# Optimization experiments

Measured on AMD Instinct MI355X. Metric: run time of the kernel, lower is better.

## Reference

```python
import jax, jax.numpy as jnp
import numpy as np

EPS = 1e-5  # nn.LayerNorm default
H = 16      # n_heads

def _ln(x, s, b):
    m = x.mean(-1, keepdims=True)
    v = x.var(-1, keepdims=True)
    return (x - m) / jnp.sqrt(v + EPS) * s + b


def setup_inputs() -> dict:
    key = jax.random.key(0)
    B, T, D, L, V = 2, 1024, 1024, 6, 32000
    ks = jax.random.split(key, 10)
    def n(k, shape):
        return jax.random.normal(k, shape, dtype=jnp.float32) * 0.02
    return dict(
        x=jax.random.randint(ks[0], (B, T), 0, V),
        tok_emb=n(ks[1], (V, D)),
        pos_emb=n(ks[2], (T, D)),
        Wq=n(ks[3], (L, D, D)), bq=jnp.zeros((L, D), jnp.float32),
        Wk=n(ks[4], (L, D, D)), bk=jnp.zeros((L, D), jnp.float32),
        Wv=n(ks[5], (L, D, D)), bv=jnp.zeros((L, D), jnp.float32),
        ln1_s=jnp.ones((L, D), jnp.float32), ln1_b=jnp.zeros((L, D), jnp.float32),
        W1=n(ks[6], (L, D, 4 * D)), b1=jnp.zeros((L, 4 * D), jnp.float32),
        W2=n(ks[7], (L, 4 * D, D)), b2=jnp.zeros((L, D), jnp.float32),
        ln2_s=jnp.ones((L, D), jnp.float32), ln2_b=jnp.zeros((L, D), jnp.float32),
        Wout=n(ks[8], (D, V)), bout=jnp.zeros((V,), jnp.float32),
    )


def reference(x, tok_emb, pos_emb, Wq, bq, Wk, bk, Wv, bv, ln1_s, ln1_b,
              W1, b1, W2, b2, ln2_s, ln2_b, Wout, bout):
    B, T = x.shape
    D = tok_emb.shape[1]
    hd = D // H
    # embeddings (dropout = identity in eval)
    h = tok_emb[x] + pos_emb[:T]
    # additive causal mask: +1.0 on allowed (tril ones kept), -inf elsewhere,
    # exactly matching torch's tril-ones masked_fill mask
    tril = jnp.tril(jnp.ones((T, T), dtype=h.dtype))
    mask = jnp.where(tril == 0, -jnp.inf, 1.0).astype(h.dtype)
    scale = jnp.asarray(1.0 / np.sqrt(hd), h.dtype)

    def block(h, p):
        wq, bq_, wk, bk_, wv, bv_, l1s, l1b, w1, b1_, w2, b2_, l2s, l2b = p
        def heads(W, b):  # [B,T,D] -> [B,H,T,hd]
            return (h @ W + b).reshape(B, T, H, hd).transpose(0, 2, 1, 3)
        q, k, v = heads(wq, bq_), heads(wk, bk_), heads(wv, bv_)
        s = jnp.einsum('bhqd,bhkd->bhqk', q, k) * scale + mask
        a = jax.nn.softmax(s, axis=-1)
        o = jnp.einsum('bhqk,bhkd->bhqd', a, v).transpose(0, 2, 1, 3).reshape(B, T, D)
        hi = _ln(o + h, l1s, l1b)
        f = jax.nn.relu(hi @ w1 + b1_) @ w2 + b2_
        return _ln(f + hi, l2s, l2b), None

    h, _ = jax.lax.scan(block, h, (Wq, bq, Wk, bk, Wv, bv, ln1_s, ln1_b,
                                   W1, b1, W2, b2, ln2_s, ln2_b))
    return h @ Wout + bout
```

## Files before the change

kernel.cpp:

```cpp
#include <hip/hip_runtime.h>
#include <cstdint>
#include <cstddef>

typedef short bf16x8 __attribute__((ext_vector_type(8)));
typedef float f32x4 __attribute__((ext_vector_type(4)));
typedef unsigned short us4 __attribute__((ext_vector_type(4)));

#define DEV static __device__ __forceinline__

DEV unsigned short f2bf(float f) {
  union { float f; unsigned u; } v; v.f = f;
  unsigned r = v.u + 0x7FFFu + ((v.u >> 16) & 1u);
  return (unsigned short)(r >> 16);
}

DEV void gll16(const void* g, void* l) {
  __builtin_amdgcn_global_load_lds((const __attribute__((address_space(1))) void*)g,
                                   (__attribute__((address_space(3))) void*)l,
                                   16, 0, 0);
}

__global__ __launch_bounds__(256) void embed_kernel(
    const int* __restrict__ x, const float* __restrict__ te,
    const float* __restrict__ pe, float* __restrict__ hf,
    unsigned short* __restrict__ hb) {
  int row = blockIdx.x;
  int t = row & 1023;
  int tok = x[row];
  int tid = threadIdx.x;
  float4 v = ((const float4*)(te + (size_t)tok * 1024))[tid];
  float4 p = ((const float4*)(pe + (size_t)t * 1024))[tid];
  v.x += p.x; v.y += p.y; v.z += p.z; v.w += p.w;
  ((float4*)(hf + (size_t)row * 1024))[tid] = v;
  us4 bv; bv[0] = f2bf(v.x); bv[1] = f2bf(v.y); bv[2] = f2bf(v.z); bv[3] = f2bf(v.w);
  ((us4*)(hb + (size_t)row * 1024))[tid] = bv;
}

__global__ __launch_bounds__(256) void wconv_kernel(
    const float* __restrict__ W, unsigned short* __restrict__ Wt, int K, int N) {
  __shared__ float tile[32][33];
  int n0 = blockIdx.x * 32, k0 = blockIdx.y * 32;
  int tx = threadIdx.x & 31, ty = threadIdx.x >> 5;
#pragma unroll
  for (int i = 0; i < 4; ++i)
    tile[ty * 4 + i][tx] = W[(size_t)(k0 + ty * 4 + i) * N + n0 + tx];
  __syncthreads();
#pragma unroll
  for (int i = 0; i < 4; ++i)
    Wt[(size_t)(n0 + ty * 4 + i) * K + k0 + tx] = f2bf(tile[tx][ty * 4 + i]);
}

__global__ __launch_bounds__(256) void wconv5_kernel(
    const float* __restrict__ Wqf, const float* __restrict__ Wkf,
    const float* __restrict__ Wvf, const float* __restrict__ W1f,
    const float* __restrict__ W2f, unsigned short* __restrict__ wsc) {
  __shared__ float tile[32][33];
  const int bid = blockIdx.x;
  const float* W; unsigned short* Wt; int K, N, b;
  if (bid < 3072) {
    const int s = bid >> 10; b = bid & 1023;
    W = s == 0 ? Wqf : (s == 1 ? Wkf : Wvf);
    Wt = wsc + (size_t)s * 1048576; K = 1024; N = 1024;
  } else if (bid < 7168) {
    b = bid - 3072; W = W1f; Wt = wsc + 3145728; K = 1024; N = 4096;
  } else {
    b = bid - 7168; W = W2f; Wt = wsc + 7340032; K = 4096; N = 1024;
  }
  const int nb = N >> 5;
  const int n0 = (b & (nb - 1)) * 32, k0 = (b / nb) * 32;
  const int tx = threadIdx.x & 31, ty = threadIdx.x >> 5;
#pragma unroll
  for (int i = 0; i < 4; ++i)
    tile[ty * 4 + i][tx] = W[(size_t)(k0 + ty * 4 + i) * N + n0 + tx];
  __syncthreads();
#pragma unroll
  for (int i = 0; i < 4; ++i)
    Wt[(size_t)(n0 + ty * 4 + i) * K + k0 + tx] = f2bf(tile[tx][ty * 4 + i]);
}

template <int EPI>
__global__ __launch_bounds__(512) void gemm5_kernel(
    const unsigned short* __restrict__ A, const unsigned short* __restrict__ Bt,
    const float* __restrict__ bias1, const float* __restrict__ bias2,
    const float* __restrict__ bias3, void* __restrict__ C1,
    void* __restrict__ C2, void* __restrict__ C3,
    int M, int N, int Kstride, int klen, int nbm) {
  constexpr int BM = 256, BN = 128, BK = 64;
  __shared__ unsigned short lA[BM * BK];
  __shared__ unsigned short lB[BN * BK];
  const int tid = threadIdx.x;
  const int wid = tid >> 6, lane = tid & 63;
  const int g = lane >> 4, c = lane & 15;
  const int wm = wid >> 1, wn = wid & 1;

  const int nwg = gridDim.x;
  const int q = nwg >> 3, r = nwg & 7;
  const int xcd = blockIdx.x & 7, jj = blockIdx.x >> 3;
  const int wgid = (xcd < r) ? (xcd * (q + 1) + jj)
                             : (r * (q + 1) + (xcd - r) * q + jj);
  const int bm = (wgid % nbm) * BM;
  const int bn = (wgid / nbm) * BN;
  const int k0 = blockIdx.z * klen;

  f32x4 acc[4][4];
#pragma unroll
  for (int mi = 0; mi < 4; ++mi)
#pragma unroll
    for (int ni = 0; ni < 4; ++ni) acc[mi][ni] = f32x4{0.f, 0.f, 0.f, 0.f};

  for (int kb = 0; kb < klen; kb += BK) {
#pragma unroll
    for (int it = 0; it < 4; ++it) {
      int chunk = it * 512 + tid;
      int row = chunk >> 3, cr = chunk & 7;
      int sc = cr ^ (row & 7);
      gll16(A + (size_t)(bm + row) * Kstride + k0 + kb + sc * 8,
            lA + (size_t)(it * 512 + wid * 64) * 8);
    }
#pragma unroll
    for (int it = 0; it < 2; ++it) {
      int chunk = it * 512 + tid;
      int row = chunk >> 3, cr = chunk & 7;
      int sc = cr ^ (row & 7);
      gll16(Bt + (size_t)(bn + row) * Kstride + k0 + kb + sc * 8,
            lB + (size_t)(it * 512 + wid * 64) * 8);
    }
    __syncthreads();
#pragma unroll
    for (int kk = 0; kk < 2; ++kk) {
      bf16x8 af[4], bfr[4];
#pragma unroll
      for (int mi = 0; mi < 4; ++mi) {
        int row = wm * 64 + mi * 16 + c;
        int ch = (kk * 4 + g) ^ (row & 7);
        af[mi] = *(const bf16x8*)(lA + row * BK + ch * 8);
      }
#pragma unroll
      for (int ni = 0; ni < 4; ++ni) {
        int row = wn * 64 + ni * 16 + c;
        int ch = (kk * 4 + g) ^ (row & 7);
        bfr[ni] = *(const bf16x8*)(lB + row * BK + ch * 8);
      }
#pragma unroll
      for (int mi = 0; mi < 4; ++mi)
#pragma unroll
        for (int ni = 0; ni < 4; ++ni)
          acc[mi][ni] = __builtin_amdgcn_mfma_f32_16x16x32_bf16(
              af[mi], bfr[ni], acc[mi][ni], 0, 0, 0);
    }
    __syncthreads();
  }

  const bool z0 = (blockIdx.z == 0);
#pragma unroll
  for (int mi = 0; mi < 4; ++mi) {
    const int row0 = bm + wm * 64 + mi * 16 + g * 4;
#pragma unroll
    for (int ni = 0; ni < 4; ++ni) {
      const int col = bn + wn * 64 + ni * 16 + c;
      if constexpr (EPI == 0) {
        float* C = z0 ? (float*)C1 : (float*)C2;
        const float bv = z0 ? bias1[col] : 0.f;
#pragma unroll
        for (int rr = 0; rr < 4; ++rr)
          C[(size_t)(row0 + rr) * N + col] = acc[mi][ni][rr] + bv;
      } else if constexpr (EPI == 2) {
        const float bv = bias1[col];
#pragma unroll
        for (int rr = 0; rr < 4; ++rr)
          ((unsigned short*)C1)[(size_t)(row0 + rr) * N + col] =
              f2bf(fmaxf(acc[mi][ni][rr] + bv, 0.f));
      } else {
        if (col < 1024) {
          const float bv = bias1[col];
#pragma unroll
          for (int rr = 0; rr < 4; ++rr)
            ((unsigned short*)C1)[(size_t)(row0 + rr) * 1024 + col] =
                f2bf(acc[mi][ni][rr] + bv);
        } else if (col < 2048) {
          const float bv = bias2[col - 1024];
#pragma unroll
          for (int rr = 0; rr < 4; ++rr)
            ((unsigned short*)C2)[(size_t)(row0 + rr) * 1024 + (col - 1024)] =
                f2bf(acc[mi][ni][rr] + bv);
        } else {
          const int cp = col - 2048;
          const float bv = bias3[cp];
          const int hh = cp >> 6, hd = cp & 63;
#pragma unroll
          for (int rr = 0; rr < 4; ++rr) {
            const int row = row0 + rr;
            const int b = row >> 10, t = row & 1023;
            ((unsigned short*)C3)[(size_t)((b * 16 + hh) * 64 + hd) * 1024 + t] =
                f2bf(acc[mi][ni][rr] + bv);
          }
        }
      }
    }
  }
}

__global__ __launch_bounds__(256) void attn_kernel(
    const unsigned short* __restrict__ q, const unsigned short* __restrict__ k,
    const unsigned short* __restrict__ vt, float* __restrict__ o) {
  __shared__ unsigned short lK[64 * 64];
  __shared__ unsigned short lV[64 * 64];
  __shared__ unsigned short lP[4][16 * 64];
  const int tid = threadIdx.x, wid = tid >> 6, lane = tid & 63;
  const int g = lane >> 4, c = lane & 15;
  const int qb = blockIdx.x * 64;
  const int h = blockIdx.y;
  const int b = blockIdx.z;
  const int qw = qb + wid * 16;

  bf16x8 aq[2];
#pragma unroll
  for (int kk = 0; kk < 2; ++kk)
    aq[kk] = *(const bf16x8*)(q + (size_t)(b * 1024 + qw + c) * 1024 + h * 64 + kk * 32 + g * 8);

  float m_run[4], l_run[4];
  f32x4 acc_o[4];
#pragma unroll
  for (int rr = 0; rr < 4; ++rr) { m_run[rr] = -INFINITY; l_run[rr] = 0.f; }
#pragma unroll
  for (int ni = 0; ni < 4; ++ni) acc_o[ni] = f32x4{0.f, 0.f, 0.f, 0.f};

  const int ntiles = qb / 64 + 1;
  for (int kt = 0; kt < ntiles; ++kt) {
#pragma unroll
    for (int it = 0; it < 2; ++it) {
      int chunk = it * 256 + tid;
      int row = chunk >> 3, cr = chunk & 7;
      int sc = cr ^ (row & 7);
      gll16(k + (size_t)(b * 1024 + kt * 64 + row) * 1024 + h * 64 + sc * 8,
            lK + (size_t)(it * 256 + wid * 64) * 8);
      gll16(vt + (size_t)((b * 16 + h) * 64 + row) * 1024 + kt * 64 + sc * 8,
            lV + (size_t)(it * 256 + wid * 64) * 8);
    }
    __syncthreads();

    f32x4 accs[4];
#pragma unroll
    for (int ni = 0; ni < 4; ++ni) accs[ni] = f32x4{0.f, 0.f, 0.f, 0.f};
#pragma unroll
    for (int kk = 0; kk < 2; ++kk)
#pragma unroll
      for (int ni = 0; ni < 4; ++ni) {
        int row = ni * 16 + c;
        int ch = (kk * 4 + g) ^ (row & 7);
        bf16x8 kf = *(const bf16x8*)(lK + row * 64 + ch * 8);
        accs[ni] = __builtin_amdgcn_mfma_f32_16x16x32_bf16(aq[kk], kf, accs[ni], 0, 0, 0);
      }

    const bool diag = (kt == qb / 64);
    float p[4][4], rowmax[4];
#pragma unroll
    for (int rr = 0; rr < 4; ++rr) rowmax[rr] = -INFINITY;
#pragma unroll
    for (int ni = 0; ni < 4; ++ni)
#pragma unroll
      for (int rr = 0; rr < 4; ++rr) {
        float s = accs[ni][rr] * 0.125f;
        if (diag) {
          int ktok = kt * 64 + ni * 16 + c;
          int qtok = qw + g * 4 + rr;
          if (ktok > qtok) s = -INFINITY;
        }
        p[ni][rr] = s;
        rowmax[rr] = fmaxf(rowmax[rr], s);
      }
#pragma unroll
    for (int mm = 1; mm < 16; mm <<= 1)
#pragma unroll
      for (int rr = 0; rr < 4; ++rr)
        rowmax[rr] = fmaxf(rowmax[rr], __shfl_xor(rowmax[rr], mm, 64));

    float alpha[4];
#pragma unroll
    for (int rr = 0; rr < 4; ++rr) {
      float mn = fmaxf(m_run[rr], rowmax[rr]);
      alpha[rr] = __expf(m_run[rr] - mn);
      m_run[rr] = mn;
    }
#pragma unroll
    for (int ni = 0; ni < 4; ++ni)
#pragma unroll
      for (int rr = 0; rr < 4; ++rr) p[ni][rr] = __expf(p[ni][rr] - m_run[rr]);

    float rowsum[4];
#pragma unroll
    for (int rr = 0; rr < 4; ++rr)
      rowsum[rr] = p[0][rr] + p[1][rr] + p[2][rr] + p[3][rr];
#pragma unroll
    for (int mm = 1; mm < 16; mm <<= 1)
#pragma unroll
      for (int rr = 0; rr < 4; ++rr) rowsum[rr] += __shfl_xor(rowsum[rr], mm, 64);
#pragma unroll
    for (int rr = 0; rr < 4; ++rr) l_run[rr] = l_run[rr] * alpha[rr] + rowsum[rr];
#pragma unroll
    for (int ni = 0; ni < 4; ++ni)
#pragma unroll
      for (int rr = 0; rr < 4; ++rr) acc_o[ni][rr] *= alpha[rr];

#pragma unroll
    for (int ni = 0; ni < 4; ++ni)
#pragma unroll
      for (int rr = 0; rr < 4; ++rr) {
        int qrow = g * 4 + rr;
        int tok = ni * 16 + c;
        int ch = (tok >> 3) ^ (qrow & 7);
        lP[wid][qrow * 64 + ch * 8 + (tok & 7)] = f2bf(p[ni][rr]);
      }

#pragma unroll
    for (int kk = 0; kk < 2; ++kk) {
      int chp = (kk * 4 + g) ^ (c & 7);
      bf16x8 pa = *(const bf16x8*)(&lP[wid][c * 64 + chp * 8]);
#pragma unroll
      for (int ni = 0; ni < 4; ++ni) {
        int row = ni * 16 + c;
        int ch = (kk * 4 + g) ^ (row & 7);
        bf16x8 vf = *(const bf16x8*)(lV + row * 64 + ch * 8);
        acc_o[ni] = __builtin_amdgcn_mfma_f32_16x16x32_bf16(pa, vf, acc_o[ni], 0, 0, 0);
      }
    }
    __syncthreads();
  }

#pragma unroll
  for (int ni = 0; ni < 4; ++ni)
#pragma unroll
    for (int rr = 0; rr < 4; ++rr) {
      int row = b * 1024 + qw + g * 4 + rr;
      int col = h * 64 + ni * 16 + c;
      o[(size_t)row * 1024 + col] = acc_o[ni][rr] / l_run[rr];
    }
}

template <int NIN>
__global__ __launch_bounds__(256) void ln_add_kernel(
    const float* __restrict__ a, const float* __restrict__ a2,
    const float* __restrict__ res,
    const float* __restrict__ s, const float* __restrict__ bb,
    float* __restrict__ out_f, unsigned short* __restrict__ out_b) {
  int row = blockIdx.x, tid = threadIdx.x;
  float4 x = ((const float4*)(a + (size_t)row * 1024))[tid];
  float4 rv = ((const float4*)(res + (size_t)row * 1024))[tid];
  x.x += rv.x; x.y += rv.y; x.z += rv.z; x.w += rv.w;
  if constexpr (NIN == 3) {
    float4 x2 = ((const float4*)(a2 + (size_t)row * 1024))[tid];
    x.x += x2.x; x.y += x2.y; x.z += x2.z; x.w += x2.w;
  }
  float sum = x.x + x.y + x.z + x.w;
  float sq = x.x * x.x + x.y * x.y + x.z * x.z + x.w * x.w;
#pragma unroll
  for (int mm = 1; mm < 64; mm <<= 1) {
    sum += __shfl_xor(sum, mm, 64);
    sq += __shfl_xor(sq, mm, 64);
  }
  __shared__ float ssum[4], ssq[4];
  int wid = tid >> 6, lane = tid & 63;
  if (lane == 0) { ssum[wid] = sum; ssq[wid] = sq; }
  __syncthreads();
  sum = ssum[0] + ssum[1] + ssum[2] + ssum[3];
  sq = ssq[0] + ssq[1] + ssq[2] + ssq[3];
  float mean = sum * (1.f / 1024.f);
  float var = sq * (1.f / 1024.f) - mean * mean;
  float rstd = rsqrtf(var + 1e-5f);
  float4 sv = ((const float4*)s)[tid];
  float4 bv = ((const float4*)bb)[tid];
  float4 y;
  y.x = (x.x - mean) * rstd * sv.x + bv.x;
  y.y = (x.y - mean) * rstd * sv.y + bv.y;
  y.z = (x.z - mean) * rstd * sv.z + bv.z;
  y.w = (x.w - mean) * rstd * sv.w + bv.w;
  ((float4*)(out_f + (size_t)row * 1024))[tid] = y;
  us4 ob; ob[0] = f2bf(y.x); ob[1] = f2bf(y.y); ob[2] = f2bf(y.z); ob[3] = f2bf(y.w);
  ((us4*)(out_b + (size_t)row * 1024))[tid] = ob;
}

extern "C" void kernel_launch(void* const* d_in, const int* in_sizes, int n_in,
                              void* d_out, int out_size, void* d_ws, size_t ws_size,
                              hipStream_t stream) {
  const int D = 1024, DFF = 4096, V = 32000, L = 6;
  const int* x = (const int*)d_in[0];
  const float* tok_emb = (const float*)d_in[1];
  const float* pos_emb = (const float*)d_in[2];
  const float* Wq = (const float*)d_in[3];  const float* bq = (const float*)d_in[4];
  const float* Wk = (const float*)d_in[5];  const float* bk = (const float*)d_in[6];
  const float* Wv = (const float*)d_in[7];  const float* bv = (const float*)d_in[8];
  const float* ln1s = (const float*)d_in[9];  const float* ln1b = (const float*)d_in[10];
  const float* W1 = (const float*)d_in[11];  const float* b1 = (const float*)d_in[12];
  const float* W2 = (const float*)d_in[13];  const float* b2 = (const float*)d_in[14];
  const float* ln2s = (const float*)d_in[15]; const float* ln2b = (const float*)d_in[16];
  const float* Wout = (const float*)d_in[17]; const float* bout = (const float*)d_in[18];

  char* ws = (char*)d_ws;
  float* h_res = (float*)(ws + 0);
  float* hi_res = (float*)(ws + 8388608);
  float* tmp = (float*)(ws + 16777216);
  unsigned short* hbf = (unsigned short*)(ws + 25165824);
  unsigned short* qb_ = (unsigned short*)(ws + 29360128);
  unsigned short* kb_ = (unsigned short*)(ws + 33554432);
  unsigned short* vtb = (unsigned short*)(ws + 37748736);
  unsigned short* ffn1 = (unsigned short*)(ws + 41943040);
  unsigned short* wsc = (unsigned short*)(ws + 58720256);
  float* tmp2 = (float*)(ws + 58720256 + 25165824);

  embed_kernel<<<2048, 256, 0, stream>>>(x, tok_emb, pos_emb, h_res, hbf);

  for (int l = 0; l < L; ++l) {
    wconv5_kernel<<<11264, 256, 0, stream>>>(
        Wq + (size_t)l * D * D, Wk + (size_t)l * D * D, Wv + (size_t)l * D * D,
        W1 + (size_t)l * D * DFF, W2 + (size_t)l * DFF * D, wsc);
    gemm5_kernel<4><<<192, 512, 0, stream>>>(
        hbf, wsc, bq + l * D, bk + l * D, bv + l * D, qb_, kb_, vtb,
        2048, 3072, D, D, 8);
    attn_kernel<<<dim3(16, 16, 2), 256, 0, stream>>>(qb_, kb_, vtb, tmp);
    ln_add_kernel<2><<<2048, 256, 0, stream>>>(
        tmp, nullptr, h_res, ln1s + l * D, ln1b + l * D, hi_res, hbf);
    gemm5_kernel<2><<<256, 512, 0, stream>>>(
        hbf, wsc + 3145728, b1 + l * DFF, nullptr, nullptr, ffn1, nullptr, nullptr,
        2048, DFF, D, D, 8);
    gemm5_kernel<0><<<dim3(64, 1, 2), 512, 0, stream>>>(
        ffn1, wsc + 7340032, b2 + l * D, nullptr, nullptr, tmp, tmp2, nullptr,
        2048, D, DFF, 2048, 8);
    ln_add_kernel<3><<<2048, 256, 0, stream>>>(
        tmp, tmp2, hi_res, ln2s + l * D, ln2b + l * D, h_res, hbf);
  }

  wconv_kernel<<<dim3(1000, 32), 256, 0, stream>>>(Wout, wsc, D, V);
  gemm5_kernel<0><<<2000, 512, 0, stream>>>(
      hbf, wsc, bout, nullptr, nullptr, (float*)d_out, nullptr, nullptr,
      2048, V, D, D, 8);
}
```

Before: 1.252 ms.

## Fuse fp32 weight conversion into GEMM B-tile loads and widen FFN2 split-K

```diff
diff --git a/kernel.cpp b/kernel.cpp
--- a/kernel.cpp
+++ b/kernel.cpp
@@ -36,55 +36,15 @@
   ((us4*)(hb + (size_t)row * 1024))[tid] = bv;
 }
 
-__global__ __launch_bounds__(256) void wconv_kernel(
-    const float* __restrict__ W, unsigned short* __restrict__ Wt, int K, int N) {
-  __shared__ float tile[32][33];
-  int n0 = blockIdx.x * 32, k0 = blockIdx.y * 32;
-  int tx = threadIdx.x & 31, ty = threadIdx.x >> 5;
-#pragma unroll
-  for (int i = 0; i < 4; ++i)
-    tile[ty * 4 + i][tx] = W[(size_t)(k0 + ty * 4 + i) * N + n0 + tx];
-  __syncthreads();
-#pragma unroll
-  for (int i = 0; i < 4; ++i)
-    Wt[(size_t)(n0 + ty * 4 + i) * K + k0 + tx] = f2bf(tile[tx][ty * 4 + i]);
-}
-
-__global__ __launch_bounds__(256) void wconv5_kernel(
-    const float* __restrict__ Wqf, const float* __restrict__ Wkf,
-    const float* __restrict__ Wvf, const float* __restrict__ W1f,
-    const float* __restrict__ W2f, unsigned short* __restrict__ wsc) {
-  __shared__ float tile[32][33];
-  const int bid = blockIdx.x;
-  const float* W; unsigned short* Wt; int K, N, b;
-  if (bid < 3072) {
-    const int s = bid >> 10; b = bid & 1023;
-    W = s == 0 ? Wqf : (s == 1 ? Wkf : Wvf);
-    Wt = wsc + (size_t)s * 1048576; K = 1024; N = 1024;
-  } else if (bid < 7168) {
-    b = bid - 3072; W = W1f; Wt = wsc + 3145728; K = 1024; N = 4096;
-  } else {
-    b = bid - 7168; W = W2f; Wt = wsc + 7340032; K = 4096; N = 1024;
-  }
-  const int nb = N >> 5;
-  const int n0 = (b & (nb - 1)) * 32, k0 = (b / nb) * 32;
-  const int tx = threadIdx.x & 31, ty = threadIdx.x >> 5;
-#pragma unroll
-  for (int i = 0; i < 4; ++i)
-    tile[ty * 4 + i][tx] = W[(size_t)(k0 + ty * 4 + i) * N + n0 + tx];
-  __syncthreads();
-#pragma unroll
-  for (int i = 0; i < 4; ++i)
-    Wt[(size_t)(n0 + ty * 4 + i) * K + k0 + tx] = f2bf(tile[tx][ty * 4 + i]);
-}
-
 template <int EPI>
-__global__ __launch_bounds__(512) void gemm5_kernel(
-    const unsigned short* __restrict__ A, const unsigned short* __restrict__ Bt,
+__global__ __launch_bounds__(512) void gemmw_kernel(
+    const unsigned short* __restrict__ A,
+    const float* __restrict__ Wa, const float* __restrict__ Wb,
+    const float* __restrict__ Wc,
     const float* __restrict__ bias1, const float* __restrict__ bias2,
     const float* __restrict__ bias3, void* __restrict__ C1,
     void* __restrict__ C2, void* __restrict__ C3,
-    int M, int N, int Kstride, int klen, int nbm) {
+    int M, int N, int Kstride, int klen, int nbm, int Nw) {
   constexpr int BM = 256, BN = 128, BK = 64;
   __shared__ unsigned short lA[BM * BK];
   __shared__ unsigned short lB[BN * BK];
@@ -102,6 +62,20 @@
   const int bn = (wgid / nbm) * BN;
   const int k0 = blockIdx.z * klen;
 
+  const float* Wsel; int ncol;
+  if constexpr (EPI == 4) {
+    const int seg = bn >> 10;
+    Wsel = seg == 0 ? Wa : (seg == 1 ? Wb : Wc);
+    ncol = bn & 1023;
+  } else {
+    Wsel = Wa; ncol = bn;
+  }
+
+  const int kch = tid >> 6;
+  const int n2 = (tid & 63) * 2;
+  const int slot0 = (kch ^ (n2 & 7)) * 8;
+  const int slot1 = (kch ^ ((n2 + 1) & 7)) * 8;
+
   f32x4 acc[4][4];
 #pragma unroll
   for (int mi = 0; mi < 4; ++mi)
@@ -117,13 +91,20 @@
       gll16(A + (size_t)(bm + row) * Kstride + k0 + kb + sc * 8,
             lA + (size_t)(it * 512 + wid * 64) * 8);
     }
-#pragma unroll
-    for (int it = 0; it < 2; ++it) {
-      int chunk = it * 512 + tid;
-      int row = chunk >> 3, cr = chunk & 7;
-      int sc = cr ^ (row & 7);
-      gll16(Bt + (size_t)(bn + row) * Kstride + k0 + kb + sc * 8,
-            lB + (size_t)(it * 512 + wid * 64) * 8);
+    {
+      const float* src = Wsel + (size_t)(k0 + kb + kch * 8) * Nw + ncol + n2;
+      float2 v[8];
+#pragma unroll
+      for (int j = 0; j < 8; ++j)
+        v[j] = *(const float2*)(src + (size_t)j * Nw);
+      bf16x8 p0, p1;
+#pragma unroll
+      for (int j = 0; j < 8; ++j) {
+        p0[j] = (short)f2bf(v[j].x);
+        p1[j] = (short)f2bf(v[j].y);
+      }
+      *(bf16x8*)(lB + n2 * BK + slot0) = p0;
+      *(bf16x8*)(lB + (n2 + 1) * BK + slot1) = p1;
     }
     __syncthreads();
 #pragma unroll
@@ -159,7 +140,7 @@
     for (int ni = 0; ni < 4; ++ni) {
       const int col = bn + wn * 64 + ni * 16 + c;
       if constexpr (EPI == 0) {
-        float* C = z0 ? (float*)C1 : (float*)C2;
+        float* C = (float*)C1 + (size_t)blockIdx.z * M * N;
         const float bv = z0 ? bias1[col] : 0.f;
 #pragma unroll
         for (int rr = 0; rr < 4; ++rr)
@@ -337,18 +318,18 @@
     }
 }
 
-template <int NIN>
+template <int NP>
 __global__ __launch_bounds__(256) void ln_add_kernel(
-    const float* __restrict__ a, const float* __restrict__ a2,
-    const float* __restrict__ res,
+    const float* __restrict__ a1, const float* __restrict__ res,
     const float* __restrict__ s, const float* __restrict__ bb,
     float* __restrict__ out_f, unsigned short* __restrict__ out_b) {
   int row = blockIdx.x, tid = threadIdx.x;
-  float4 x = ((const float4*)(a + (size_t)row * 1024))[tid];
+  float4 x = ((const float4*)(a1 + (size_t)row * 1024))[tid];
   float4 rv = ((const float4*)(res + (size_t)row * 1024))[tid];
   x.x += rv.x; x.y += rv.y; x.z += rv.z; x.w += rv.w;
-  if constexpr (NIN == 3) {
-    float4 x2 = ((const float4*)(a2 + (size_t)row * 1024))[tid];
+#pragma unroll
+  for (int pimg = 1; pimg < NP; ++pimg) {
+    float4 x2 = ((const float4*)(a1 + (size_t)pimg * 2097152 + (size_t)row * 1024))[tid];
     x.x += x2.x; x.y += x2.y; x.z += x2.z; x.w += x2.w;
   }
   float sum = x.x + x.y + x.z + x.w;
@@ -398,39 +379,36 @@
   char* ws = (char*)d_ws;
   float* h_res = (float*)(ws + 0);
   float* hi_res = (float*)(ws + 8388608);
-  float* tmp = (float*)(ws + 16777216);
-  unsigned short* hbf = (unsigned short*)(ws + 25165824);
-  unsigned short* qb_ = (unsigned short*)(ws + 29360128);
-  unsigned short* kb_ = (unsigned short*)(ws + 33554432);
-  unsigned short* vtb = (unsigned short*)(ws + 37748736);
-  unsigned short* ffn1 = (unsigned short*)(ws + 41943040);
-  unsigned short* wsc = (unsigned short*)(ws + 58720256);
-  float* tmp2 = (float*)(ws + 58720256 + 25165824);
+  unsigned short* hbf = (unsigned short*)(ws + 16777216);
+  unsigned short* qb_ = (unsigned short*)(ws + 20971520);
+  unsigned short* kb_ = (unsigned short*)(ws + 25165824);
+  unsigned short* vtb = (unsigned short*)(ws + 29360128);
+  unsigned short* ffn1 = (unsigned short*)(ws + 33554432);
+  float* part = (float*)(ws + 50331648);
 
   embed_kernel<<<2048, 256, 0, stream>>>(x, tok_emb, pos_emb, h_res, hbf);
 
   for (int l = 0; l < L; ++l) {
-    wconv5_kernel<<<11264, 256, 0, stream>>>(
-        Wq + (size_t)l * D * D, Wk + (size_t)l * D * D, Wv + (size_t)l * D * D,
-        W1 + (size_t)l * D * DFF, W2 + (size_t)l * DFF * D, wsc);
-    gemm5_kernel<4><<<192, 512, 0, stream>>>(
-        hbf, wsc, bq + l * D, bk + l * D, bv + l * D, qb_, kb_, vtb,
-        2048, 3072, D, D, 8);
-    attn_kernel<<<dim3(16, 16, 2), 256, 0, stream>>>(qb_, kb_, vtb, tmp);
-    ln_add_kernel<2><<<2048, 256, 0, stream>>>(
-        tmp, nullptr, h_res, ln1s + l * D, ln1b + l * D, hi_res, hbf);
-    gemm5_kernel<2><<<256, 512, 0, stream>>>(
-        hbf, wsc + 3145728, b1 + l * DFF, nullptr, nullptr, ffn1, nullptr, nullptr,
-        2048, DFF, D, D, 8);
-    gemm5_kernel<0><<<dim3(64, 1, 2), 512, 0, stream>>>(
-        ffn1, wsc + 7340032, b2 + l * D, nullptr, nullptr, tmp, tmp2, nullptr,
-        2048, D, DFF, 2048, 8);
-    ln_add_kernel<3><<<2048, 256, 0, stream>>>(
-        tmp, tmp2, hi_res, ln2s + l * D, ln2b + l * D, h_res, hbf);
-  }
-
-  wconv_kernel<<<dim3(1000, 32), 256, 0, stream>>>(Wout, wsc, D, V);
-  gemm5_kernel<0><<<2000, 512, 0, stream>>>(
-      hbf, wsc, bout, nullptr, nullptr, (float*)d_out, nullptr, nullptr,
-      2048, V, D, D, 8);
-}
+    gemmw_kernel<4><<<192, 512, 0, stream>>>(
+        hbf, Wq + (size_t)l * D * D, Wk + (size_t)l * D * D, Wv + (size_t)l * D * D,
+        bq + l * D, bk + l * D, bv + l * D, qb_, kb_, vtb,
+        2048, 3072, D, D, 8, D);
+    attn_kernel<<<dim3(16, 16, 2), 256, 0, stream>>>(qb_, kb_, vtb, part);
+    ln_add_kernel<1><<<2048, 256, 0, stream>>>(
+        part, h_res, ln1s + l * D, ln1b + l * D, hi_res, hbf);
+    gemmw_kernel<2><<<256, 512, 0, stream>>>(
+        hbf, W1 + (size_t)l * D * DFF, nullptr, nullptr,
+        b1 + l * DFF, nullptr, nullptr, ffn1, nullptr, nullptr,
+        2048, DFF, D, D, 8, DFF);
+    gemmw_kernel<0><<<dim3(64, 1, 4), 512, 0, stream>>>(
+        ffn1, W2 + (size_t)l * DFF * D, nullptr, nullptr,
+        b2 + l * D, nullptr, nullptr, part, nullptr, nullptr,
+        2048, D, DFF, 1024, 8, D);
+    ln_add_kernel<4><<<2048, 256, 0, stream>>>(
+        part, hi_res, ln2s + l * D, ln2b + l * D, h_res, hbf);
+  }
+
+  gemmw_kernel<0><<<2000, 512, 0, stream>>>(
+      hbf, Wout, nullptr, nullptr, bout, nullptr, nullptr,
+      (float*)d_out, nullptr, nullptr, 2048, V, D, D, 8, V);
+}
```

After: 1.345 ms. 7.4% more time.

## Use 128-key attention tiles and 4-way split-K for the FFN down projection

Applied to the files above, without the earlier changes.

```diff
diff --git a/kernel.cpp b/kernel.cpp
--- a/kernel.cpp
+++ b/kernel.cpp
@@ -159,7 +159,7 @@
     for (int ni = 0; ni < 4; ++ni) {
       const int col = bn + wn * 64 + ni * 16 + c;
       if constexpr (EPI == 0) {
-        float* C = z0 ? (float*)C1 : (float*)C2;
+        float* C = (float*)C1 + (size_t)blockIdx.z * M * N;
         const float bv = z0 ? bias1[col] : 0.f;
 #pragma unroll
         for (int rr = 0; rr < 4; ++rr)
@@ -203,9 +203,9 @@
 __global__ __launch_bounds__(256) void attn_kernel(
     const unsigned short* __restrict__ q, const unsigned short* __restrict__ k,
     const unsigned short* __restrict__ vt, float* __restrict__ o) {
-  __shared__ unsigned short lK[64 * 64];
-  __shared__ unsigned short lV[64 * 64];
-  __shared__ unsigned short lP[4][16 * 64];
+  __shared__ unsigned short lK[128 * 64];
+  __shared__ unsigned short lV[64 * 128];
+  __shared__ unsigned short lP[4][16 * 128];
   const int tid = threadIdx.x, wid = tid >> 6, lane = tid & 63;
   const int g = lane >> 4, c = lane & 15;
   const int qb = blockIdx.x * 64;
@@ -225,44 +225,52 @@
 #pragma unroll
   for (int ni = 0; ni < 4; ++ni) acc_o[ni] = f32x4{0.f, 0.f, 0.f, 0.f};
 
-  const int ntiles = qb / 64 + 1;
+  const int ntiles = (qb >> 7) + 1;
   for (int kt = 0; kt < ntiles; ++kt) {
 #pragma unroll
-    for (int it = 0; it < 2; ++it) {
+    for (int it = 0; it < 4; ++it) {
       int chunk = it * 256 + tid;
       int row = chunk >> 3, cr = chunk & 7;
       int sc = cr ^ (row & 7);
-      gll16(k + (size_t)(b * 1024 + kt * 64 + row) * 1024 + h * 64 + sc * 8,
+      gll16(k + (size_t)(b * 1024 + kt * 128 + row) * 1024 + h * 64 + sc * 8,
             lK + (size_t)(it * 256 + wid * 64) * 8);
-      gll16(vt + (size_t)((b * 16 + h) * 64 + row) * 1024 + kt * 64 + sc * 8,
+    }
+#pragma unroll
+    for (int it = 0; it < 4; ++it) {
+      int chunk = it * 256 + tid;
+      int row = chunk >> 4, cr = chunk & 15;
+      int sc = cr ^ (row & 7);
+      gll16(vt + (size_t)((b * 16 + h) * 64 + row) * 1024 + kt * 128 + sc * 8,
             lV + (size_t)(it * 256 + wid * 64) * 8);
     }
     __syncthreads();
 
-    f32x4 accs[4];
-#pragma unroll
-    for (int ni = 0; ni < 4; ++ni) accs[ni] = f32x4{0.f, 0.f, 0.f, 0.f};
+    f32x4 accs[8];
+#pragma unroll
+    for (int ni = 0; ni < 8; ++ni) accs[ni] = f32x4{0.f, 0.f, 0.f, 0.f};
+    __builtin_amdgcn_s_setprio(1);
 #pragma unroll
     for (int kk = 0; kk < 2; ++kk)
 #pragma unroll
-      for (int ni = 0; ni < 4; ++ni) {
+      for (int ni = 0; ni < 8; ++ni) {
         int row = ni * 16 + c;
         int ch = (kk * 4 + g) ^ (row & 7);
         bf16x8 kf = *(const bf16x8*)(lK + row * 64 + ch * 8);
         accs[ni] = __builtin_amdgcn_mfma_f32_16x16x32_bf16(aq[kk], kf, accs[ni], 0, 0, 0);
       }
-
-    const bool diag = (kt == qb / 64);
-    float p[4][4], rowmax[4];
+    __builtin_amdgcn_s_setprio(0);
+
+    const bool diag = (kt == ntiles - 1);
+    float p[8][4], rowmax[4];
 #pragma unroll
     for (int rr = 0; rr < 4; ++rr) rowmax[rr] = -INFINITY;
 #pragma unroll
-    for (int ni = 0; ni < 4; ++ni)
+    for (int ni = 0; ni < 8; ++ni)
 #pragma unroll
       for (int rr = 0; rr < 4; ++rr) {
         float s = accs[ni][rr] * 0.125f;
         if (diag) {
-          int ktok = kt * 64 + ni * 16 + c;
+          int ktok = kt * 128 + ni * 16 + c;
           int qtok = qw + g * 4 + rr;
           if (ktok > qtok) s = -INFINITY;
         }
@@ -283,47 +291,51 @@
       m_run[rr] = mn;
     }
 #pragma unroll
+    for (int ni = 0; ni < 8; ++ni)
+#pragma unroll
+      for (int rr = 0; rr < 4; ++rr) p[ni][rr] = __expf(p[ni][rr] - m_run[rr]);
+
+    float rowsum[4];
+#pragma unroll
+    for (int rr = 0; rr < 4; ++rr)
+      rowsum[rr] = ((p[0][rr] + p[1][rr]) + (p[2][rr] + p[3][rr])) +
+                   ((p[4][rr] + p[5][rr]) + (p[6][rr] + p[7][rr]));
+#pragma unroll
+    for (int mm = 1; mm < 16; mm <<= 1)
+#pragma unroll
+      for (int rr = 0; rr < 4; ++rr) rowsum[rr] += __shfl_xor(rowsum[rr], mm, 64);
+#pragma unroll
+    for (int rr = 0; rr < 4; ++rr) l_run[rr] = l_run[rr] * alpha[rr] + rowsum[rr];
+#pragma unroll
     for (int ni = 0; ni < 4; ++ni)
 #pragma unroll
-      for (int rr = 0; rr < 4; ++rr) p[ni][rr] = __expf(p[ni][rr] - m_run[rr]);
-
-    float rowsum[4];
-#pragma unroll
-    for (int rr = 0; rr < 4; ++rr)
-      rowsum[rr] = p[0][rr] + p[1][rr] + p[2][rr] + p[3][rr];
-#pragma unroll
-    for (int mm = 1; mm < 16; mm <<= 1)
-#pragma unroll
-      for (int rr = 0; rr < 4; ++rr) rowsum[rr] += __shfl_xor(rowsum[rr], mm, 64);
-#pragma unroll
-    for (int rr = 0; rr < 4; ++rr) l_run[rr] = l_run[rr] * alpha[rr] + rowsum[rr];
-#pragma unroll
-    for (int ni = 0; ni < 4; ++ni)
-#pragma unroll
       for (int rr = 0; rr < 4; ++rr) acc_o[ni][rr] *= alpha[rr];
 
 #pragma unroll
-    for (int ni = 0; ni < 4; ++ni)
+    for (int ni = 0; ni < 8; ++ni)
 #pragma unroll
       for (int rr = 0; rr < 4; ++rr) {
         int qrow = g * 4 + rr;
         int tok = ni * 16 + c;
         int ch = (tok >> 3) ^ (qrow & 7);
-        lP[wid][qrow * 64 + ch * 8 + (tok & 7)] = f2bf(p[ni][rr]);
-      }
-
-#pragma unroll
-    for (int kk = 0; kk < 2; ++kk) {
-      int chp = (kk * 4 + g) ^ (c & 7);
-      bf16x8 pa = *(const bf16x8*)(&lP[wid][c * 64 + chp * 8]);
+        lP[wid][qrow * 128 + ch * 8 + (tok & 7)] = f2bf(p[ni][rr]);
+      }
+
+    __builtin_amdgcn_s_setprio(1);
+#pragma unroll
+    for (int kk = 0; kk < 4; ++kk) {
+      int kc = kk * 4 + g;
+      int chp = kc ^ (c & 7);
+      bf16x8 pa = *(const bf16x8*)(&lP[wid][c * 128 + chp * 8]);
 #pragma unroll
       for (int ni = 0; ni < 4; ++ni) {
         int row = ni * 16 + c;
-        int ch = (kk * 4 + g) ^ (row & 7);
-        bf16x8 vf = *(const bf16x8*)(lV + row * 64 + ch * 8);
+        int ch = kc ^ (row & 7);
+        bf16x8 vf = *(const bf16x8*)(lV + row * 128 + ch * 8);
         acc_o[ni] = __builtin_amdgcn_mfma_f32_16x16x32_bf16(pa, vf, acc_o[ni], 0, 0, 0);
       }
     }
+    __builtin_amdgcn_s_setprio(0);
     __syncthreads();
   }
 
@@ -337,18 +349,18 @@
     }
 }
 
-template <int NIN>
+template <int NP>
 __global__ __launch_bounds__(256) void ln_add_kernel(
-    const float* __restrict__ a, const float* __restrict__ a2,
-    const float* __restrict__ res,
+    const float* __restrict__ a1, const float* __restrict__ res,
     const float* __restrict__ s, const float* __restrict__ bb,
     float* __restrict__ out_f, unsigned short* __restrict__ out_b) {
   int row = blockIdx.x, tid = threadIdx.x;
-  float4 x = ((const float4*)(a + (size_t)row * 1024))[tid];
+  float4 x = ((const float4*)(a1 + (size_t)row * 1024))[tid];
   float4 rv = ((const float4*)(res + (size_t)row * 1024))[tid];
   x.x += rv.x; x.y += rv.y; x.z += rv.z; x.w += rv.w;
-  if constexpr (NIN == 3) {
-    float4 x2 = ((const float4*)(a2 + (size_t)row * 1024))[tid];
+#pragma unroll
+  for (int pimg = 1; pimg < NP; ++pimg) {
+    float4 x2 = ((const float4*)(a1 + (size_t)pimg * 2097152 + (size_t)row * 1024))[tid];
     x.x += x2.x; x.y += x2.y; x.z += x2.z; x.w += x2.w;
   }
   float sum = x.x + x.y + x.z + x.w;
@@ -405,7 +417,7 @@
   unsigned short* vtb = (unsigned short*)(ws + 37748736);
   unsigned short* ffn1 = (unsigned short*)(ws + 41943040);
   unsigned short* wsc = (unsigned short*)(ws + 58720256);
-  float* tmp2 = (float*)(ws + 58720256 + 25165824);
+  float* part = (float*)(ws + 58720256 + 25165824);
 
   embed_kernel<<<2048, 256, 0, stream>>>(x, tok_emb, pos_emb, h_res, hbf);
 
@@ -417,16 +429,16 @@
         hbf, wsc, bq + l * D, bk + l * D, bv + l * D, qb_, kb_, vtb,
         2048, 3072, D, D, 8);
     attn_kernel<<<dim3(16, 16, 2), 256, 0, stream>>>(qb_, kb_, vtb, tmp);
-    ln_add_kernel<2><<<2048, 256, 0, stream>>>(
-        tmp, nullptr, h_res, ln1s + l * D, ln1b + l * D, hi_res, hbf);
+    ln_add_kernel<1><<<2048, 256, 0, stream>>>(
+        tmp, h_res, ln1s + l * D, ln1b + l * D, hi_res, hbf);
     gemm5_kernel<2><<<256, 512, 0, stream>>>(
         hbf, wsc + 3145728, b1 + l * DFF, nullptr, nullptr, ffn1, nullptr, nullptr,
         2048, DFF, D, D, 8);
-    gemm5_kernel<0><<<dim3(64, 1, 2), 512, 0, stream>>>(
-        ffn1, wsc + 7340032, b2 + l * D, nullptr, nullptr, tmp, tmp2, nullptr,
-        2048, D, DFF, 2048, 8);
-    ln_add_kernel<3><<<2048, 256, 0, stream>>>(
-        tmp, tmp2, hi_res, ln2s + l * D, ln2b + l * D, h_res, hbf);
+    gemm5_kernel<0><<<dim3(64, 1, 4), 512, 0, stream>>>(
+        ffn1, wsc + 7340032, b2 + l * D, nullptr, nullptr, part, nullptr, nullptr,
+        2048, D, DFF, 1024, 8);
+    ln_add_kernel<4><<<2048, 256, 0, stream>>>(
+        part, hi_res, ln2s + l * D, ln2b + l * D, h_res, hbf);
   }
 
   wconv_kernel<<<dim3(1000, 32), 256, 0, stream>>>(Wout, wsc, D, V);
```

Measured after the change: 1.155 ms. 1.08x faster.
